# Kernel tuning notes

Hardware: AMD Instinct MI355X
Metric: run time of the kernel (lower is better)

Reference implementation:

```python
import jax, jax.numpy as jnp
import numpy as np

DMODEL = 65  # module-level constant in the source, used for both proj width and scale
DK = DQ = DV = 64
B, L = 8, 4096


def setup_inputs() -> dict:
    key = jax.random.key(0)
    ks = jax.random.split(key, 7)
    s = 1.0 / np.sqrt(DMODEL)
    return {
        "x":  jax.random.normal(ks[0], (B, L, DMODEL), dtype=jnp.float32),
        "Wq": jax.random.uniform(ks[1], (DMODEL, DQ), jnp.float32, -s, s),
        "bq": jax.random.uniform(ks[2], (DQ,), jnp.float32, -s, s),
        "Wk": jax.random.uniform(ks[3], (DMODEL, DK), jnp.float32, -s, s),
        "bk": jax.random.uniform(ks[4], (DK,), jnp.float32, -s, s),
        "Wv": jax.random.uniform(ks[5], (DMODEL, DV), jnp.float32, -s, s),
        "bv": jax.random.uniform(ks[6], (DV,), jnp.float32, -s, s),
    }


def reference(x, Wq, bq, Wk, bk, Wv, bv):
    # QKV projections (single head)
    q = x @ Wq + bq            # [B, L, DQ]
    k = x @ Wk + bk            # [B, L, DK]
    v = x @ Wv + bv            # [B, L, DV]
    # scaled dot-product scores; source scales by sqrt(dmodel)=sqrt(65)
    scores = jnp.einsum("bqd,bkd->bqk", q, k) / (DMODEL ** 0.5)  # [B, L, L]
    # causal mask (intended semantics of the source's tril-based masked_fill)
    causal = jnp.tril(jnp.ones((L, L), dtype=bool))
    scores = jnp.where(causal, scores, jnp.float32(-jnp.inf))
    probs = jax.nn.softmax(scores, axis=-1)  # dropout omitted (eval mode)
    return probs @ v           # [B, L, DV]
```

## Files before the change

kernel.cpp:

```cpp
#include <hip/hip_runtime.h>
#include <hip/hip_bf16.h>

#define B_  8
#define L_  4096
#define DH  64

typedef __attribute__((ext_vector_type(8)))  __bf16 bf16x8;
typedef __attribute__((ext_vector_type(16))) float  f32x16;
typedef __attribute__((ext_vector_type(4)))  float  f32x4;
typedef __attribute__((ext_vector_type(8)))  unsigned short u16x8;

#define QW_OFF  0u
#define KW_OFF  2097152u
#define VP_OFF  4194304u
#define OP_OFF  6291456u
#define LP_OFFB 46137344u

__global__ __launch_bounds__(256) void qkv_proj(
    const float* __restrict__ x,
    const float* __restrict__ Wq, const float* __restrict__ bq,
    const float* __restrict__ Wk, const float* __restrict__ bk,
    const float* __restrict__ Wv, const float* __restrict__ bv,
    unsigned short* __restrict__ qo,
    unsigned short* __restrict__ Kp,
    unsigned short* __restrict__ Vp)
{
    __shared__ __align__(16) unsigned short xs[64 * 104];
    __shared__ __align__(16) unsigned short wt[64 * 104];
    __shared__ __align__(16) unsigned short bounce[64 * 64];
    __shared__ float bsm[64];

    const int tid = threadIdx.x;
    const int r0  = blockIdx.x * 64;
    const int bb  = r0 >> 12;
    const int l0  = r0 & 4095;

    {
        const u16x8 z = {0,0,0,0,0,0,0,0};
        for (int i = tid; i < (64 * 104) / 8; i += 256) {
            ((u16x8*)xs)[i] = z;  ((u16x8*)wt)[i] = z;
        }
    }
    __syncthreads();

    for (int i = tid; i < 64 * 65; i += 256) {
        const int row = i / 65, col = i - row * 65;
        __hip_bfloat16 v = __float2bfloat16(x[(size_t)r0 * 65 + i]);
        xs[row * 104 + col] = *(unsigned short*)&v;
    }

    const float* Wp[3] = {Wq, Wk, Wv};
    const float* bp[3] = {bq, bk, bv};

    const int w = tid >> 6, lane = tid & 63, li = lane & 15, lg = lane >> 4;
    const int rb = w * 16;

#pragma unroll
    for (int p = 0; p < 3; ++p) {
        __syncthreads();
        for (int i = tid; i < 65 * 64; i += 256) {
            const int k = i >> 6, cc = i & 63;
            __hip_bfloat16 v = __float2bfloat16(Wp[p][i]);
            wt[cc * 104 + k] = *(unsigned short*)&v;
        }
        if (tid < 64) bsm[tid] = bp[p][tid];
        __syncthreads();

        f32x4 acc[4];
#pragma unroll
        for (int j = 0; j < 4; ++j) {
            const float bv_ = bsm[j * 16 + li];
            acc[j] = (f32x4){bv_, bv_, bv_, bv_};
        }
#pragma unroll
        for (int ks = 0; ks < 3; ++ks) {
            const bf16x8 a = __builtin_bit_cast(bf16x8,
                *(const u16x8*)&xs[(rb + li) * 104 + ks * 32 + 8 * lg]);
#pragma unroll
            for (int j = 0; j < 4; ++j) {
                const bf16x8 bf = __builtin_bit_cast(bf16x8,
                    *(const u16x8*)&wt[(j * 16 + li) * 104 + ks * 32 + 8 * lg]);
                acc[j] = __builtin_amdgcn_mfma_f32_16x16x32_bf16(a, bf, acc[j], 0, 0, 0);
            }
        }

        const float scale = (p == 0) ? (1.4426950408889634f / 8.06225774829855f) : 1.0f;
#pragma unroll
        for (int j = 0; j < 4; ++j)
#pragma unroll
            for (int r = 0; r < 4; ++r) {
                __hip_bfloat16 hv = __float2bfloat16(acc[j][r] * scale);
                bounce[(rb + lg * 4 + r) * 64 + j * 16 + li] = *(unsigned short*)&hv;
            }
        __syncthreads();

        if (p == 0) {
            const int row = tid >> 2, col = (tid & 3) * 16;
            unsigned short* op = qo + (size_t)(r0 + row) * 64 + col;
            *(u16x8*)op       = *(const u16x8*)&bounce[row * 64 + col];
            *(u16x8*)(op + 8) = *(const u16x8*)&bounce[row * 64 + col + 8];
        } else if (p == 1) {
#pragma unroll
            for (int e = 0; e < 2; ++e) {
                const int pi = tid * 2 + e;
                const int row = pi >> 3, s = pi & 7;
                const int l = l0 + row;
                const u16x8 piece = *(const u16x8*)&bounce[row * 64 + ((s ^ (row & 7)) << 3)];
                *(u16x8*)(Kp + (size_t)(bb * 128 + (l >> 5)) * 2048 + (l & 31) * 64 + s * 8) = piece;
            }
        } else {
#pragma unroll
            for (int e = 0; e < 2; ++e) {
                const int pi = tid * 2 + e;
                const int t32 = pi >> 8, rem = pi & 255;
                const int dv = rem >> 2, cp = rem & 3;
                const int u = cp ^ ((dv >> 1) & 3);
                const int m = u >> 1, h = u & 1;
                u16x8 piece;
#pragma unroll
                for (int j = 0; j < 8; ++j) {
                    const int kv = m * 16 + h * 4 + (j & 3) + 8 * (j >> 2);
                    piece[j] = bounce[(t32 * 32 + kv) * 64 + dv];
                }
                *(u16x8*)(Vp + (size_t)(bb * 128 + (l0 >> 5) + t32) * 2048 + dv * 32 + cp * 8) = piece;
            }
        }
    }
}

__global__ __launch_bounds__(256, 4) void attn(
    const unsigned short* __restrict__ Q,
    const unsigned short* __restrict__ Kp,
    const unsigned short* __restrict__ Vp,
    float* __restrict__ O,
    unsigned short* __restrict__ Op,
    float* __restrict__ Lp)
{
    __shared__ __align__(16) unsigned short SM[2][8192];

    const int tid  = threadIdx.x;
    const int w    = tid >> 6;
    const int lane = tid & 63;
    const int li32 = lane & 31;
    const int h    = lane >> 5;

    const int b = blockIdx.x & 7;
    const int p = 143 - (blockIdx.x >> 3);
    int g = 0;
    while (2 * (g + 1) * (g + 2) <= p) ++g;
    const int id2 = p - 2 * g * (g + 1);
    const int qq  = id2 / (g + 1);
    const int qb  = 4 * g + qq;
    const int c   = id2 - qq * (g + 1);

    const int q0    = qb * 128;
    const int kv0   = c << 9;
    const int kvend = (kv0 + 512 < q0 + 128) ? kv0 + 512 : q0 + 128;
    const int ntl   = (kvend - kv0) >> 6;
    const int q0w   = q0 + w * 32;
    const int q     = q0w + li32;

    const size_t base = (size_t)b * L_ * DH;
    const unsigned short* KpB = Kp + ((size_t)(b * 128) + (kv0 >> 5)) * 2048;
    const unsigned short* VpB = Vp + ((size_t)(b * 128) + (kv0 >> 5)) * 2048;

    auto stage_t = [&](int buf, int t) {
        const unsigned short* ksrc = KpB + (size_t)t * 4096 + w * 512 + lane * 8;
        const unsigned short* vsrc = VpB + (size_t)t * 4096 + w * 512 + lane * 8;
        unsigned short* kdst = &SM[buf][0]    + w * 512;
        unsigned short* vdst = &SM[buf][4096] + w * 512;
#pragma unroll
        for (int j2 = 0; j2 < 2; ++j2) {
            __builtin_amdgcn_global_load_lds(
                (const __attribute__((address_space(1))) void*)(ksrc + j2 * 2048),
                (__attribute__((address_space(3))) void*)(kdst + j2 * 2048), 16, 0, 0);
            __builtin_amdgcn_global_load_lds(
                (const __attribute__((address_space(1))) void*)(vsrc + j2 * 2048),
                (__attribute__((address_space(3))) void*)(vdst + j2 * 2048), 16, 0, 0);
        }
    };

    stage_t(0, 0);
    if (ntl > 1) stage_t(1, 1);

    bf16x8 qf[4];
#pragma unroll
    for (int ks = 0; ks < 4; ++ks)
        qf[ks] = __builtin_bit_cast(bf16x8,
            *(const u16x8*)(Q + base + (size_t)q * DH + ks * 16 + h * 8));

    u16x8 ou;
#pragma unroll
    for (int i = 0; i < 8; ++i) ou[i] = 0x3F80;
    const bf16x8 ones = __builtin_bit_cast(bf16x8, ou);

    f32x16 o0, o1, l_acc;
#pragma unroll
    for (int r = 0; r < 16; ++r) { o0[r] = 0.0f; o1[r] = 0.0f; l_acc[r] = 0.0f; }

    for (int t = 0; t < ntl; ++t) {
        if (t + 1 < ntl) { asm volatile("s_waitcnt vmcnt(4)" ::: "memory"); }
        else             { asm volatile("s_waitcnt vmcnt(0)" ::: "memory"); }
        __builtin_amdgcn_s_barrier();

        const int kvb = kv0 + t * 64;
        const unsigned short* SMp = &SM[t & 1][0];

        if (kvb <= q0w + 31) {
#pragma unroll
            for (int sub = 0; sub < 2; ++sub) {
                const int kvbs = kvb + sub * 32;
                if (sub == 1 && kvbs > q0w + 31) break;
                const int soff = sub * 2048;

                f32x16 s;
#pragma unroll
                for (int r = 0; r < 16; ++r) s[r] = -8.0f;
                __builtin_amdgcn_s_setprio(1);
#pragma unroll
                for (int ks = 0; ks < 4; ++ks) {
                    const bf16x8 kf = __builtin_bit_cast(bf16x8,
                        *(const u16x8*)&SMp[soff + li32 * 64 +
                                            ((((ks << 1) | h) ^ (li32 & 7)) << 3)]);
                    s = __builtin_amdgcn_mfma_f32_32x32x16_bf16(kf, qf[ks], s, 0, 0, 0);
                }
                __builtin_amdgcn_s_setprio(0);

                if (kvbs + 31 > q0w) {
#pragma unroll
                    for (int r = 0; r < 16; ++r) {
                        const int kv = kvbs + (r & 3) + ((r >> 2) << 3) + (h << 2);
                        s[r] = (kv > q) ? -1e30f : s[r];
                    }
                }

#pragma unroll
                for (int r = 0; r < 16; ++r) s[r] = __builtin_amdgcn_exp2f(s[r]);

                bf16x8 pf0, pf1;
#pragma unroll
                for (int i = 0; i < 8; ++i) {
                    pf0[i] = (__bf16)s[i];
                    pf1[i] = (__bf16)s[8 + i];
                }

                __builtin_amdgcn_s_setprio(1);
                l_acc = __builtin_amdgcn_mfma_f32_32x32x16_bf16(pf0, ones, l_acc, 0, 0, 0);
                l_acc = __builtin_amdgcn_mfma_f32_32x32x16_bf16(pf1, ones, l_acc, 0, 0, 0);

                {
                    const int dv = li32;
                    const int c0 = ((0 | h) ^ ((dv >> 1) & 3)) << 3;
                    const int c1 = ((2 | h) ^ ((dv >> 1) & 3)) << 3;
                    const bf16x8 v0 = __builtin_bit_cast(bf16x8,
                        *(const u16x8*)&SMp[4096 + soff + dv * 32 + c0]);
                    const bf16x8 v1 = __builtin_bit_cast(bf16x8,
                        *(const u16x8*)&SMp[4096 + soff + dv * 32 + c1]);
                    o0 = __builtin_amdgcn_mfma_f32_32x32x16_bf16(pf0, v0, o0, 0, 0, 0);
                    o0 = __builtin_amdgcn_mfma_f32_32x32x16_bf16(pf1, v1, o0, 0, 0, 0);
                }
                {
                    const int dv = 32 + li32;
                    const int c0 = ((0 | h) ^ ((dv >> 1) & 3)) << 3;
                    const int c1 = ((2 | h) ^ ((dv >> 1) & 3)) << 3;
                    const bf16x8 v0 = __builtin_bit_cast(bf16x8,
                        *(const u16x8*)&SMp[4096 + soff + dv * 32 + c0]);
                    const bf16x8 v1 = __builtin_bit_cast(bf16x8,
                        *(const u16x8*)&SMp[4096 + soff + dv * 32 + c1]);
                    o1 = __builtin_amdgcn_mfma_f32_32x32x16_bf16(pf0, v0, o1, 0, 0, 0);
                    o1 = __builtin_amdgcn_mfma_f32_32x32x16_bf16(pf1, v1, o1, 0, 0, 0);
                }
                __builtin_amdgcn_s_setprio(0);
            }
        }

        __builtin_amdgcn_s_barrier();
        if (t + 2 < ntl) stage_t(t & 1, t + 2);
    }

    if (g == 0) {
#pragma unroll
        for (int r = 0; r < 16; ++r) {
            const int row = (r & 3) + ((r >> 2) << 3) + (h << 2);
            const float inv = 1.0f / l_acc[r];
            float* orow = O + ((size_t)b * L_ + q0w + row) * DH;
            orow[li32]      = o0[r] * inv;
            orow[32 + li32] = o1[r] * inv;
        }
    } else {
        const int idx = (b * 32 + qb) * 8 + c;
        unsigned short* po = Op + (size_t)idx * 8192;
        float* lp = Lp + (size_t)idx * 128;
#pragma unroll
        for (int r = 0; r < 16; ++r) {
            const int row = (r & 3) + ((r >> 2) << 3) + (h << 2);
            __hip_bfloat16 h0 = __float2bfloat16(o0[r]);
            __hip_bfloat16 h1 = __float2bfloat16(o1[r]);
            po[(w * 32 + row) * 64 + li32]      = *(unsigned short*)&h0;
            po[(w * 32 + row) * 64 + 32 + li32] = *(unsigned short*)&h1;
            if (li32 == 0) lp[w * 32 + row] = l_acc[r];
        }
    }
}

__global__ __launch_bounds__(256) void merge(
    const unsigned short* __restrict__ Op,
    const float* __restrict__ Lp,
    float* __restrict__ O)
{
    const int b  = blockIdx.x & 7;
    const int qb = 4 + (blockIdx.x >> 3);
    const int nc = (qb >> 2) + 1;

    const int row = threadIdx.x >> 1;
    const int c0  = (threadIdx.x & 1) * 32;
    const int idx0 = (b * 32 + qb) * 8;

    float acc[32];
#pragma unroll
    for (int j = 0; j < 32; ++j) acc[j] = 0.0f;
    float Lr = 0.0f;

    for (int cc = 0; cc < nc; ++cc) {
        Lr += Lp[(size_t)(idx0 + cc) * 128 + row];
        const unsigned short* pp = Op + (size_t)(idx0 + cc) * 8192 + row * 64 + c0;
#pragma unroll
        for (int j8 = 0; j8 < 4; ++j8) {
            const u16x8 a = *(const u16x8*)(pp + j8 * 8);
#pragma unroll
            for (int j = 0; j < 8; ++j) {
                const unsigned int ua = ((unsigned int)a[j]) << 16;
                acc[j8 * 8 + j] += __builtin_bit_cast(float, ua);
            }
        }
    }

    const float inv = 1.0f / Lr;
    float* out = O + ((size_t)b * L_ + qb * 128 + row) * DH + c0;
#pragma unroll
    for (int j4 = 0; j4 < 8; ++j4) {
        f32x4 v;
#pragma unroll
        for (int j = 0; j < 4; ++j) v[j] = acc[j4 * 4 + j] * inv;
        *(f32x4*)(out + j4 * 4) = v;
    }
}

extern "C" void kernel_launch(void* const* d_in, const int* in_sizes, int n_in,
                              void* d_out, int out_size, void* d_ws, size_t ws_size,
                              hipStream_t stream)
{
    const float* x  = (const float*)d_in[0];
    const float* Wq = (const float*)d_in[1];
    const float* bq = (const float*)d_in[2];
    const float* Wk = (const float*)d_in[3];
    const float* bk = (const float*)d_in[4];
    const float* Wv = (const float*)d_in[5];
    const float* bv = (const float*)d_in[6];

    unsigned short* ws16 = (unsigned short*)d_ws;
    unsigned short* qw  = ws16 + QW_OFF;
    unsigned short* kp  = ws16 + KW_OFF;
    unsigned short* vp  = ws16 + VP_OFF;
    unsigned short* Opp = ws16 + OP_OFF;
    float* Lp = (float*)((char*)d_ws + LP_OFFB);

    qkv_proj<<<512, 256, 0, stream>>>(x, Wq, bq, Wk, bk, Wv, bv, qw, kp, vp);
    attn<<<1152, 256, 0, stream>>>(qw, kp, vp, (float*)d_out, Opp, Lp);
    merge<<<224, 256, 0, stream>>>(Opp, Lp, (float*)d_out);
}
```

Baseline: 54.56 us.

## Process two 32-row query tiles per wave with 128-thread attention blocks

The attention kernel now runs 2 waves per block instead of 4, and each wave handles 64 query rows as two 32-row subtiles. The K fragments loaded from LDS and the V fragments are reused across both subtiles, which halves LDS read traffic per query row. Each wave also issues twice as many global-to-LDS loads, with the wait count adjusted to match. The cost is higher register pressure from six accumulators and fewer waves per block, which may reduce latency hiding and occupancy.

```diff
diff --git a/kernel.cpp b/kernel.cpp
--- a/kernel.cpp
+++ b/kernel.cpp
@@ -128,7 +128,7 @@
     }
 }
 
-__global__ __launch_bounds__(256, 4) void attn(
+__global__ __launch_bounds__(128, 2) void attn(
     const unsigned short* __restrict__ Q,
     const unsigned short* __restrict__ Kp,
     const unsigned short* __restrict__ Vp,
@@ -157,118 +157,143 @@
     const int kv0   = c << 9;
     const int kvend = (kv0 + 512 < q0 + 128) ? kv0 + 512 : q0 + 128;
     const int ntl   = (kvend - kv0) >> 6;
-    const int q0w   = q0 + w * 32;
-    const int q     = q0w + li32;
+    const int q0w   = q0 + w * 64;
 
     const size_t base = (size_t)b * L_ * DH;
     const unsigned short* KpB = Kp + ((size_t)(b * 128) + (kv0 >> 5)) * 2048;
     const unsigned short* VpB = Vp + ((size_t)(b * 128) + (kv0 >> 5)) * 2048;
 
     auto stage_t = [&](int buf, int t) {
-        const unsigned short* ksrc = KpB + (size_t)t * 4096 + w * 512 + lane * 8;
-        const unsigned short* vsrc = VpB + (size_t)t * 4096 + w * 512 + lane * 8;
-        unsigned short* kdst = &SM[buf][0]    + w * 512;
-        unsigned short* vdst = &SM[buf][4096] + w * 512;
-#pragma unroll
-        for (int j2 = 0; j2 < 2; ++j2) {
+        const unsigned short* kt = KpB + (size_t)t * 4096 + w * 2048 + lane * 8;
+        const unsigned short* vt = VpB + (size_t)t * 4096 + w * 2048 + lane * 8;
+        unsigned short* kd = &SM[buf][0]    + w * 2048;
+        unsigned short* vd = &SM[buf][4096] + w * 2048;
+#pragma unroll
+        for (int j = 0; j < 4; ++j) {
             __builtin_amdgcn_global_load_lds(
-                (const __attribute__((address_space(1))) void*)(ksrc + j2 * 2048),
-                (__attribute__((address_space(3))) void*)(kdst + j2 * 2048), 16, 0, 0);
+                (const __attribute__((address_space(1))) void*)(kt + j * 512),
+                (__attribute__((address_space(3))) void*)(kd + j * 512), 16, 0, 0);
             __builtin_amdgcn_global_load_lds(
-                (const __attribute__((address_space(1))) void*)(vsrc + j2 * 2048),
-                (__attribute__((address_space(3))) void*)(vdst + j2 * 2048), 16, 0, 0);
+                (const __attribute__((address_space(1))) void*)(vt + j * 512),
+                (__attribute__((address_space(3))) void*)(vd + j * 512), 16, 0, 0);
         }
     };
 
     stage_t(0, 0);
     if (ntl > 1) stage_t(1, 1);
 
-    bf16x8 qf[4];
-#pragma unroll
-    for (int ks = 0; ks < 4; ++ks)
-        qf[ks] = __builtin_bit_cast(bf16x8,
-            *(const u16x8*)(Q + base + (size_t)q * DH + ks * 16 + h * 8));
+    bf16x8 qf[2][4];
+#pragma unroll
+    for (int i = 0; i < 2; ++i)
+#pragma unroll
+        for (int ks = 0; ks < 4; ++ks)
+            qf[i][ks] = __builtin_bit_cast(bf16x8,
+                *(const u16x8*)(Q + base + (size_t)(q0w + i * 32 + li32) * DH
+                                + ks * 16 + h * 8));
 
     u16x8 ou;
 #pragma unroll
     for (int i = 0; i < 8; ++i) ou[i] = 0x3F80;
     const bf16x8 ones = __builtin_bit_cast(bf16x8, ou);
 
-    f32x16 o0, o1, l_acc;
-#pragma unroll
-    for (int r = 0; r < 16; ++r) { o0[r] = 0.0f; o1[r] = 0.0f; l_acc[r] = 0.0f; }
+    f32x16 o00, o01, o10, o11, l0a, l1a;
+#pragma unroll
+    for (int r = 0; r < 16; ++r) {
+        o00[r] = 0.0f; o01[r] = 0.0f; o10[r] = 0.0f; o11[r] = 0.0f;
+        l0a[r] = 0.0f; l1a[r] = 0.0f;
+    }
 
     for (int t = 0; t < ntl; ++t) {
-        if (t + 1 < ntl) { asm volatile("s_waitcnt vmcnt(4)" ::: "memory"); }
+        if (t + 1 < ntl) { asm volatile("s_waitcnt vmcnt(8)" ::: "memory"); }
         else             { asm volatile("s_waitcnt vmcnt(0)" ::: "memory"); }
         __builtin_amdgcn_s_barrier();
 
-        const int kvb = kv0 + t * 64;
+        const int kvbase = kv0 + t * 64;
         const unsigned short* SMp = &SM[t & 1][0];
 
-        if (kvb <= q0w + 31) {
+        if (kvbase <= q0w + 63) {
 #pragma unroll
             for (int sub = 0; sub < 2; ++sub) {
-                const int kvbs = kvb + sub * 32;
-                if (sub == 1 && kvbs > q0w + 31) break;
+                const int kvbs = kvbase + sub * 32;
+                if (sub == 1 && kvbs > q0w + 63) break;
                 const int soff = sub * 2048;
-
-                f32x16 s;
-#pragma unroll
-                for (int r = 0; r < 16; ++r) s[r] = -8.0f;
-                __builtin_amdgcn_s_setprio(1);
-#pragma unroll
-                for (int ks = 0; ks < 4; ++ks) {
-                    const bf16x8 kf = __builtin_bit_cast(bf16x8,
+                const bool a0 = (kvbs <= q0w + 31);
+
+                bf16x8 kf[4];
+#pragma unroll
+                for (int ks = 0; ks < 4; ++ks)
+                    kf[ks] = __builtin_bit_cast(bf16x8,
                         *(const u16x8*)&SMp[soff + li32 * 64 +
                                             ((((ks << 1) | h) ^ (li32 & 7)) << 3)]);
-                    s = __builtin_amdgcn_mfma_f32_32x32x16_bf16(kf, qf[ks], s, 0, 0, 0);
+
+                f32x16 s0, s1;
+#pragma unroll
+                for (int r = 0; r < 16; ++r) { s0[r] = -8.0f; s1[r] = -8.0f; }
+                __builtin_amdgcn_s_setprio(1);
+#pragma unroll
+                for (int ks = 0; ks < 4; ++ks)
+                    s1 = __builtin_amdgcn_mfma_f32_32x32x16_bf16(kf[ks], qf[1][ks], s1, 0, 0, 0);
+                if (a0) {
+#pragma unroll
+                    for (int ks = 0; ks < 4; ++ks)
+                        s0 = __builtin_amdgcn_mfma_f32_32x32x16_bf16(kf[ks], qf[0][ks], s0, 0, 0, 0);
                 }
                 __builtin_amdgcn_s_setprio(0);
 
-                if (kvbs + 31 > q0w) {
+                if (kvbs + 31 > q0w + 32) {
+                    const int q1 = q0w + 32 + li32;
 #pragma unroll
                     for (int r = 0; r < 16; ++r) {
                         const int kv = kvbs + (r & 3) + ((r >> 2) << 3) + (h << 2);
-                        s[r] = (kv > q) ? -1e30f : s[r];
+                        s1[r] = (kv > q1) ? -1e30f : s1[r];
                     }
                 }
-
-#pragma unroll
-                for (int r = 0; r < 16; ++r) s[r] = __builtin_amdgcn_exp2f(s[r]);
-
-                bf16x8 pf0, pf1;
-#pragma unroll
-                for (int i = 0; i < 8; ++i) {
-                    pf0[i] = (__bf16)s[i];
-                    pf1[i] = (__bf16)s[8 + i];
-                }
+                if (a0 && kvbs + 31 > q0w) {
+                    const int qv = q0w + li32;
+#pragma unroll
+                    for (int r = 0; r < 16; ++r) {
+                        const int kv = kvbs + (r & 3) + ((r >> 2) << 3) + (h << 2);
+                        s0[r] = (kv > qv) ? -1e30f : s0[r];
+                    }
+                }
+
+#pragma unroll
+                for (int r = 0; r < 16; ++r) s1[r] = __builtin_amdgcn_exp2f(s1[r]);
+                bf16x8 pf1a, pf1b;
+#pragma unroll
+                for (int i = 0; i < 8; ++i) { pf1a[i] = (__bf16)s1[i]; pf1b[i] = (__bf16)s1[8 + i]; }
+                bf16x8 pf0a, pf0b;
+                if (a0) {
+#pragma unroll
+                    for (int r = 0; r < 16; ++r) s0[r] = __builtin_amdgcn_exp2f(s0[r]);
+#pragma unroll
+                    for (int i = 0; i < 8; ++i) { pf0a[i] = (__bf16)s0[i]; pf0b[i] = (__bf16)s0[8 + i]; }
+                }
+
+                const int dv0 = li32, dv1 = 32 + li32;
+                const bf16x8 v00 = __builtin_bit_cast(bf16x8,
+                    *(const u16x8*)&SMp[4096 + soff + dv0 * 32 + (((0 | h) ^ ((dv0 >> 1) & 3)) << 3)]);
+                const bf16x8 v01 = __builtin_bit_cast(bf16x8,
+                    *(const u16x8*)&SMp[4096 + soff + dv0 * 32 + (((2 | h) ^ ((dv0 >> 1) & 3)) << 3)]);
+                const bf16x8 v10 = __builtin_bit_cast(bf16x8,
+                    *(const u16x8*)&SMp[4096 + soff + dv1 * 32 + (((0 | h) ^ ((dv1 >> 1) & 3)) << 3)]);
+                const bf16x8 v11 = __builtin_bit_cast(bf16x8,
+                    *(const u16x8*)&SMp[4096 + soff + dv1 * 32 + (((2 | h) ^ ((dv1 >> 1) & 3)) << 3)]);
 
                 __builtin_amdgcn_s_setprio(1);
-                l_acc = __builtin_amdgcn_mfma_f32_32x32x16_bf16(pf0, ones, l_acc, 0, 0, 0);
-                l_acc = __builtin_amdgcn_mfma_f32_32x32x16_bf16(pf1, ones, l_acc, 0, 0, 0);
-
-                {
-                    const int dv = li32;
-                    const int c0 = ((0 | h) ^ ((dv >> 1) & 3)) << 3;
-                    const int c1 = ((2 | h) ^ ((dv >> 1) & 3)) << 3;
-                    const bf16x8 v0 = __builtin_bit_cast(bf16x8,
-                        *(const u16x8*)&SMp[4096 + soff + dv * 32 + c0]);
-                    const bf16x8 v1 = __builtin_bit_cast(bf16x8,
-                        *(const u16x8*)&SMp[4096 + soff + dv * 32 + c1]);
-                    o0 = __builtin_amdgcn_mfma_f32_32x32x16_bf16(pf0, v0, o0, 0, 0, 0);
-                    o0 = __builtin_amdgcn_mfma_f32_32x32x16_bf16(pf1, v1, o0, 0, 0, 0);
-                }
-                {
-                    const int dv = 32 + li32;
-                    const int c0 = ((0 | h) ^ ((dv >> 1) & 3)) << 3;
-                    const int c1 = ((2 | h) ^ ((dv >> 1) & 3)) << 3;
-                    const bf16x8 v0 = __builtin_bit_cast(bf16x8,
-                        *(const u16x8*)&SMp[4096 + soff + dv * 32 + c0]);
-                    const bf16x8 v1 = __builtin_bit_cast(bf16x8,
-                        *(const u16x8*)&SMp[4096 + soff + dv * 32 + c1]);
-                    o1 = __builtin_amdgcn_mfma_f32_32x32x16_bf16(pf0, v0, o1, 0, 0, 0);
-                    o1 = __builtin_amdgcn_mfma_f32_32x32x16_bf16(pf1, v1, o1, 0, 0, 0);
+                l1a = __builtin_amdgcn_mfma_f32_32x32x16_bf16(pf1a, ones, l1a, 0, 0, 0);
+                l1a = __builtin_amdgcn_mfma_f32_32x32x16_bf16(pf1b, ones, l1a, 0, 0, 0);
+                o10 = __builtin_amdgcn_mfma_f32_32x32x16_bf16(pf1a, v00, o10, 0, 0, 0);
+                o10 = __builtin_amdgcn_mfma_f32_32x32x16_bf16(pf1b, v01, o10, 0, 0, 0);
+                o11 = __builtin_amdgcn_mfma_f32_32x32x16_bf16(pf1a, v10, o11, 0, 0, 0);
+                o11 = __builtin_amdgcn_mfma_f32_32x32x16_bf16(pf1b, v11, o11, 0, 0, 0);
+                if (a0) {
+                    l0a = __builtin_amdgcn_mfma_f32_32x32x16_bf16(pf0a, ones, l0a, 0, 0, 0);
+                    l0a = __builtin_amdgcn_mfma_f32_32x32x16_bf16(pf0b, ones, l0a, 0, 0, 0);
+                    o00 = __builtin_amdgcn_mfma_f32_32x32x16_bf16(pf0a, v00, o00, 0, 0, 0);
+                    o00 = __builtin_amdgcn_mfma_f32_32x32x16_bf16(pf0b, v01, o00, 0, 0, 0);
+                    o01 = __builtin_amdgcn_mfma_f32_32x32x16_bf16(pf0a, v10, o01, 0, 0, 0);
+                    o01 = __builtin_amdgcn_mfma_f32_32x32x16_bf16(pf0b, v11, o01, 0, 0, 0);
                 }
                 __builtin_amdgcn_s_setprio(0);
             }
@@ -282,10 +307,14 @@
 #pragma unroll
         for (int r = 0; r < 16; ++r) {
             const int row = (r & 3) + ((r >> 2) << 3) + (h << 2);
-            const float inv = 1.0f / l_acc[r];
-            float* orow = O + ((size_t)b * L_ + q0w + row) * DH;
-            orow[li32]      = o0[r] * inv;
-            orow[32 + li32] = o1[r] * inv;
+            const float inv0 = 1.0f / l0a[r];
+            const float inv1 = 1.0f / l1a[r];
+            float* orow0 = O + ((size_t)b * L_ + q0w + row) * DH;
+            float* orow1 = O + ((size_t)b * L_ + q0w + 32 + row) * DH;
+            orow0[li32]      = o00[r] * inv0;
+            orow0[32 + li32] = o01[r] * inv0;
+            orow1[li32]      = o10[r] * inv1;
+            orow1[32 + li32] = o11[r] * inv1;
         }
     } else {
         const int idx = (b * 32 + qb) * 8 + c;
@@ -293,12 +322,18 @@
         float* lp = Lp + (size_t)idx * 128;
 #pragma unroll
         for (int r = 0; r < 16; ++r) {
-            const int row = (r & 3) + ((r >> 2) << 3) + (h << 2);
-            __hip_bfloat16 h0 = __float2bfloat16(o0[r]);
-            __hip_bfloat16 h1 = __float2bfloat16(o1[r]);
-            po[(w * 32 + row) * 64 + li32]      = *(unsigned short*)&h0;
-            po[(w * 32 + row) * 64 + 32 + li32] = *(unsigned short*)&h1;
-            if (li32 == 0) lp[w * 32 + row] = l_acc[r];
+            const int rr = (r & 3) + ((r >> 2) << 3) + (h << 2);
+            const int row0 = w * 64 + rr;
+            const int row1 = w * 64 + 32 + rr;
+            __hip_bfloat16 h00 = __float2bfloat16(o00[r]);
+            __hip_bfloat16 h01 = __float2bfloat16(o01[r]);
+            __hip_bfloat16 h10 = __float2bfloat16(o10[r]);
+            __hip_bfloat16 h11 = __float2bfloat16(o11[r]);
+            po[row0 * 64 + li32]      = *(unsigned short*)&h00;
+            po[row0 * 64 + 32 + li32] = *(unsigned short*)&h01;
+            po[row1 * 64 + li32]      = *(unsigned short*)&h10;
+            po[row1 * 64 + 32 + li32] = *(unsigned short*)&h11;
+            if (li32 == 0) { lp[row0] = l0a[r]; lp[row1] = l1a[r]; }
         }
     }
 }
@@ -366,6 +401,6 @@
     float* Lp = (float*)((char*)d_ws + LP_OFFB);
 
     qkv_proj<<<512, 256, 0, stream>>>(x, Wq, bq, Wk, bk, Wv, bv, qw, kp, vp);
-    attn<<<1152, 256, 0, stream>>>(qw, kp, vp, (float*)d_out, Opp, Lp);
+    attn<<<1152, 128, 0, stream>>>(qw, kp, vp, (float*)d_out, Opp, Lp);
     merge<<<224, 256, 0, stream>>>(Opp, Lp, (float*)d_out);
 }
```

Result: slower. 61.88 us (+13.4%).
